# Performance work log

Hardware: AMD Instinct MI355X
Metric: run time of the kernel (lower is better)

Reference implementation:

```python
import jax, jax.numpy as jnp
import numpy as np

P = 524288          # total sampled points
N_RAYS = 4096       # rays
N_FREQ = 5
N_FREQ_VIEW = 3
ACT_SHIFT = float(np.log(1.0 / (1.0 - 0.1) - 1.0))  # alpha_init = 0.1
INTERVAL = 0.5      # stepsize * voxel_size_ratio


def sin_emb(x, n_freq):
    # x: (M,3) -> (M, 3 + 6*n_freq): [x, sin(2^i x), cos(2^i x)]
    freqs = 2.0 ** jnp.arange(n_freq, dtype=x.dtype)
    parts = [x]
    for f in freqs:
        parts.append(jnp.sin(f * x))
        parts.append(jnp.cos(f * x))
    return jnp.concatenate(parts, axis=1)


def _pipeline(sampling_coor, sampling_view, raw_density, ray_id,
              wb0, bb0, wb1, bb1, wb2, bb2,
              wa0, ba0, wa1, ba1, wa2, ba2,
              w_lat, b_lat, w_view, b_view, w_c0, b_c0, w_c1, b_c1):
    relu = jax.nn.relu
    emb = sin_emb(sampling_coor, N_FREQ)                    # (P, 33)
    view_emb = sin_emb(sampling_view, N_FREQ_VIEW)[ray_id]  # (P, 21)
    # Decoder_woslot (K == 1)
    h = relu(emb @ wb0 + bb0)
    h = relu(h @ wb1 + bb1)
    h = relu(h @ wb2 + bb2)
    h = jnp.concatenate([emb, h], axis=1)                   # skip: (P, 97)
    h = relu(h @ wa0 + ba0)
    h = relu(h @ wa1 + ba1)
    h = relu(h @ wa2 + ba2)
    latent = h @ w_lat + b_lat                              # (P, 64)
    hv = relu(jnp.concatenate([latent, view_emb], axis=1) @ w_view + b_view)
    rgb_raw = relu(hv @ w_c0 + b_c0) @ w_c1 + b_c1          # (P, 3)
    rgb = (jnp.tanh(rgb_raw) + 1.0) * 0.5
    sigma = jax.nn.softplus(raw_density[0] + ACT_SHIFT)     # (P,)
    # Raw2Alpha: alpha = 1 - exp(-sigma*interval); hence log(1-alpha) = -sigma*interval
    alpha = 1.0 - jnp.exp(-sigma * INTERVAL)
    log_t = -sigma * INTERVAL
    # Alphas2Weights: per-ray exclusive cumprod of (1-alpha); ray_id is sorted
    cl = jnp.cumsum(log_t)
    excl = cl - log_t                                        # exclusive global cumsum
    base = jax.ops.segment_max(excl, ray_id, num_segments=N_RAYS)  # value at each ray start
    T = jnp.exp(excl - base[ray_id])                         # transmittance
    weights = T * alpha                                      # (P,)
    alphainv_last = jnp.exp(jax.ops.segment_sum(log_t, ray_id, num_segments=N_RAYS))
    # composite with white background
    rgb_marched = (jax.ops.segment_sum(weights[:, None] * rgb, ray_id, num_segments=N_RAYS)
                   + alphainv_last[:, None])
    return rgb_marched                                       # (N_RAYS, 3)


def setup_inputs() -> dict:
    key = jax.random.key(0)
    ks = iter(jax.random.split(key, 40))

    def w(fi, fo):
        return jax.random.normal(next(ks), (fi, fo), jnp.float32) / np.sqrt(fi).astype(np.float32)

    inp = {
        'sampling_coor': jax.random.normal(next(ks), (P, 3), jnp.float32),
        'sampling_view': jax.random.normal(next(ks), (N_RAYS, 3), jnp.float32),
        'raw_density': jax.random.normal(next(ks), (1, P), jnp.float32),
        'ray_id': jnp.sort(jax.random.randint(next(ks), (P,), 0, N_RAYS, jnp.int32)),
        'wb0': w(33, 64), 'bb0': jnp.zeros((64,), jnp.float32),
        'wb1': w(64, 64), 'bb1': jnp.zeros((64,), jnp.float32),
        'wb2': w(64, 64), 'bb2': jnp.zeros((64,), jnp.float32),
        'wa0': w(97, 64), 'ba0': jnp.zeros((64,), jnp.float32),
        'wa1': w(64, 64), 'ba1': jnp.zeros((64,), jnp.float32),
        'wa2': w(64, 64), 'ba2': jnp.zeros((64,), jnp.float32),
        'w_lat': w(64, 64), 'b_lat': jnp.zeros((64,), jnp.float32),
        'w_view': w(85, 32), 'b_view': jnp.zeros((32,), jnp.float32),
        'w_c0': w(32, 16), 'b_c0': jnp.zeros((16,), jnp.float32),
        'w_c1': w(16, 3), 'b_c1': jnp.zeros((3,), jnp.float32),
    }
    return inp


def reference(sampling_coor, sampling_view, raw_density, ray_id,
              wb0, bb0, wb1, bb1, wb2, bb2,
              wa0, ba0, wa1, ba1, wa2, ba2,
              w_lat, b_lat, w_view, b_view, w_c0, b_c0, w_c1, b_c1):
    return _pipeline(sampling_coor, sampling_view, raw_density, ray_id,
                     wb0, bb0, wb1, bb1, wb2, bb2,
                     wa0, ba0, wa1, ba1, wa2, ba2,
                     w_lat, b_lat, w_view, b_view, w_c0, b_c0, w_c1, b_c1)
```

## Files before the change

kernel.cpp:

```cpp
#include <hip/hip_runtime.h>
#include <math.h>

#define NPTS  524288
#define NRAYS 4096
#define ACT_SHIFT_F (-2.1972245773362196f)
#define INTERVAL_F  0.5f

typedef _Float16 f16x8  __attribute__((ext_vector_type(8)));
typedef __fp16   fp16x2 __attribute__((ext_vector_type(2)));
typedef float    f32x4  __attribute__((ext_vector_type(4)));
typedef float    f32x16 __attribute__((ext_vector_type(16)));
typedef int      i32x2  __attribute__((ext_vector_type(2)));
typedef unsigned u32;
typedef unsigned u32x2  __attribute__((ext_vector_type(2)));
typedef unsigned u32x4  __attribute__((ext_vector_type(4)));

#define MFMA32(a,b,c) __builtin_amdgcn_mfma_f32_32x32x16_f16((a),(b),(c),0,0,0)

#define WB0_H    0
#define WB1_H    3328
#define WB2_H    7680
#define WA0_H    12032
#define WA1_H    19456
#define WA2_H    23808
#define WLAT_H   28160
#define WLDS_H   32512
#define WVIEW_H  32512
#define WC0_H    35584
#define WEND_H   36608
#define BTAB_H   36608
#define VTAB_H   37376
#define RAYTAB_H 168448
#define PREP_W    36608
#define PREP_BT   (PREP_W + 384)
#define PREP_IDS  (PREP_BT + NRAYS)
#define PREP_TOTAL (PREP_IDS + NPTS)

#define S2_WB0 26
#define S2_D   34
#define S2_WA0 58
#define U_WB0  0
#define U_WB1  1664
#define U_WB2  3840
#define U_WA0  6016
#define U_WA1  9728
#define U_WA2  11904
#define U_WLAT 14080
#define LDS_U32 16256

__device__ __forceinline__ u32 pk(float a, float b) {
    fp16x2 h = __builtin_amdgcn_cvt_pkrtz(a, b);
    return __builtin_bit_cast(u32, h);
}

__device__ __forceinline__ void plswap(u32 &x, u32 &y) {
    i32x2 r = __builtin_amdgcn_permlane32_swap((int)x, (int)y, false, false);
    x = (u32)r[0]; y = (u32)r[1];
}

__device__ __forceinline__ f32x16 zero16() {
    f32x16 z;
#pragma unroll
    for (int i = 0; i < 16; ++i) z[i] = 0.f;
    return z;
}

template<bool RELU>
__device__ __forceinline__ f16x8 reluq(f16x8 v) {
    if (RELU) {
        f16x8 z = {};
        return __builtin_elementwise_max(v, z);
    }
    return v;
}

template<bool RELU>
__device__ __forceinline__ void d2b(f32x16 a, f16x8 &blo, f16x8 &bhi) {
    u32 p0 = pk(a[0],a[1]),   p1 = pk(a[2],a[3]);
    u32 p2 = pk(a[4],a[5]),   p3 = pk(a[6],a[7]);
    plswap(p0, p2); plswap(p1, p3);
    u32x4 lo = {p0, p1, p2, p3};
    blo = reluq<RELU>(__builtin_bit_cast(f16x8, lo));
    u32 p4 = pk(a[8],a[9]),   p5 = pk(a[10],a[11]);
    u32 p6 = pk(a[12],a[13]), p7 = pk(a[14],a[15]);
    plswap(p4, p6); plswap(p5, p7);
    u32x4 hw = {p4, p5, p6, p7};
    bhi = reluq<RELU>(__builtin_bit_cast(f16x8, hw));
}

__device__ __forceinline__ f16x8 ldw(const u32* __restrict__ sw, int u) {
    u32x2 a = *(const u32x2*)(sw + u);
    u32x2 b = *(const u32x2*)(sw + u + 2);
    u32x4 r = {a[0], a[1], b[0], b[1]};
    return __builtin_bit_cast(f16x8, r);
}

extern "C" __global__ void __launch_bounds__(256)
prep_weights(const float* __restrict__ wb0, const float* __restrict__ bb0,
             const float* __restrict__ wb1, const float* __restrict__ bb1,
             const float* __restrict__ wb2, const float* __restrict__ bb2,
             const float* __restrict__ wa0, const float* __restrict__ ba0,
             const float* __restrict__ wa1, const float* __restrict__ ba1,
             const float* __restrict__ wa2, const float* __restrict__ ba2,
             const float* __restrict__ wlat, const float* __restrict__ blat,
             const float* __restrict__ wview, const float* __restrict__ bview,
             const float* __restrict__ wc0, const float* __restrict__ bc0,
             const float* __restrict__ view, const int* __restrict__ ray_id,
             _Float16* __restrict__ pool)
{
    const int id = blockIdx.x * 256 + threadIdx.x;
    if (id >= PREP_TOTAL) return;

    if (id < PREP_W) {
        int r = id; float v = 0.f;
        if (r < 3328) {
            int n = r / 52, k = r % 52;
            if (k < 3) v = wb0[k*64+n]; else if (k == 3) v = bb0[n];
            else if (k < 34) v = wb0[(k-1)*64+n];
        } else if (r < 7680) { r -= 3328;
            int n = r / 68, k = r % 68; if (k < 64) v = wb1[k*64+n];
        } else if (r < 12032) { r -= 7680;
            int n = r / 68, k = r % 68; if (k < 64) v = wb2[k*64+n];
        } else if (r < 19456) { r -= 12032;
            int n = r / 116, k = r % 116;
            if (k < 3) v = wa0[k*64+n]; else if (k == 3) v = ba0[n];
            else if (k < 34) v = wa0[(k-1)*64+n];
            else if (k >= 48 && k < 112) v = wa0[(k-15)*64+n];
        } else if (r < 23808) { r -= 19456;
            int n = r / 68, k = r % 68; if (k < 64) v = wa1[k*64+n];
        } else if (r < 28160) { r -= 23808;
            int n = r / 68, k = r % 68; if (k < 64) v = wa2[k*64+n];
        } else if (r < 32512) { r -= 28160;
            int n = r / 68, k = r % 68; if (k < 64) v = wlat[k*64+n];
        } else if (r < 35584) { r -= 32512;
            int n = r / 96, k = r % 96;
            if (k < 64) v = wview[k*32+n];
            else { int s = k - 64;
                   if (s < 3) v = wview[(64+s)*32+n];
                   else if (s == 3) v = bview[n];
                   else if (s < 22) v = wview[(63+s)*32+n]; }
        } else { r -= 35584;
            int n = r >> 5, k = r & 31;
            if (n < 16) v = wc0[k*16+n];
        }
        pool[id] = (_Float16)v;
        return;
    }

    if (id < PREP_BT) {
        float* bt = (float*)(pool + BTAB_H);
        const int e = id - PREP_W; float v = 0.f;
        if (e < 320) {
            int l = e >> 6, rem = e & 63;
            int mt = rem >> 5, hi2 = (rem >> 4) & 1, q = rem & 15;
            int row = (q & 3) + 8*(q >> 2) + 4*hi2 + 32*mt;
            const float* src[5] = { bb1, bb2, ba1, ba2, blat };
            v = src[l][row];
        } else if (e < 336) {
            int t = e - 320, hi2 = t >> 3, q = t & 7;
            int row = (q & 3) + 8*(q >> 2) + 4*hi2;
            v = bc0[row];
        }
        bt[e] = v;
        return;
    }

    if (id < PREP_IDS) {
        const int ray = id - PREP_BT;
        const float vx = view[3*ray+0], vy = view[3*ray+1], vz = view[3*ray+2];
        u32 w_[16];
        w_[0] = pk(vx, vy); w_[1] = pk(vz, 1.0f);
#pragma unroll
        for (int f = 0; f < 3; ++f) {
            const float fac = (float)(1 << f);
            float sx = __sinf(fac*vx), cx = __cosf(fac*vx);
            float sy = __sinf(fac*vy), cy = __cosf(fac*vy);
            float sz = __sinf(fac*vz), cz = __cosf(fac*vz);
            w_[2+3*f+0] = pk(sx,sy); w_[2+3*f+1] = pk(sz,cx); w_[2+3*f+2] = pk(cy,cz);
        }
#pragma unroll
        for (int i = 11; i < 16; ++i) w_[i] = 0u;
        u32* dst = (u32*)(pool + VTAB_H) + ray * 16;
#pragma unroll
        for (int i = 0; i < 4; ++i)
            ((u32x4*)dst)[i] = (u32x4){w_[4*i], w_[4*i+1], w_[4*i+2], w_[4*i+3]};
        return;
    }

    {
        const int p = id - PREP_IDS;
        int* tab = (int*)(pool + RAYTAB_H);
        const int cur  = ray_id[p];
        const int prev = (p == 0) ? -1 : ray_id[p-1];
        for (int r = prev + 1; r <= cur; ++r) tab[r] = p;
        if (p == NPTS - 1)
            for (int r = cur + 1; r <= NRAYS; ++r) tab[r] = NPTS;
    }
}

__device__ __forceinline__ void loadBV(f32x16 (&bv)[2], const float* __restrict__ bt,
                                       int l, int hi) {
#pragma unroll
    for (int mt = 0; mt < 2; ++mt) {
        const float* p = bt + l*64 + (mt*2 + hi)*16;
#pragma unroll
        for (int i = 0; i < 4; ++i) {
            f32x4 v = *(const f32x4*)(p + 4*i);
#pragma unroll
            for (int s = 0; s < 4; ++s) bv[mt][4*i + s] = v[s];
        }
    }
}

template<bool RELU>
__device__ __forceinline__ void denseL(const u32* __restrict__ sw, int base,
                                       const f32x16 (&bv)[2], f16x8 (&b)[4][4],
                                       int col, int hi) {
    f16x8 W[2][4];
#pragma unroll
    for (int mt = 0; mt < 2; ++mt)
#pragma unroll
        for (int kc = 0; kc < 4; ++kc)
            W[mt][kc] = ldw(sw, base + (mt*32 + col)*S2_D + kc*8 + hi*4);
#pragma unroll
    for (int t = 0; t < 4; ++t) {
        f32x16 a0 = MFMA32(W[0][0], b[t][0], bv[0]);
        f32x16 a1 = MFMA32(W[1][0], b[t][0], bv[1]);
#pragma unroll
        for (int kc = 1; kc < 4; ++kc) {
            a0 = MFMA32(W[0][kc], b[t][kc], a0);
            a1 = MFMA32(W[1][kc], b[t][kc], a1);
        }
        d2b<RELU>(a0, b[t][0], b[t][1]);
        d2b<RELU>(a1, b[t][2], b[t][3]);
    }
}

extern "C" __global__ void __launch_bounds__(512, 2)
mlp_mfma(const float* __restrict__ coor, const int* __restrict__ ray_id,
         const float* __restrict__ wc1, const float* __restrict__ bc1,
         const _Float16* __restrict__ pool, _Float16* __restrict__ rgb)
{
    __shared__ __align__(16) u32 sw[LDS_U32];
    const int tid  = threadIdx.x;
    const int lane = tid & 63;
    const int wv   = tid >> 6;
    const int col  = lane & 31;
    const int hi   = lane >> 5;
    const int wbase = blockIdx.x * 1024 + wv * 128;

    {
        const u32x4* pw = (const u32x4*)pool;
        u32x4* dw = (u32x4*)sw;
#pragma unroll
        for (int i = tid; i < LDS_U32/4; i += 512) dw[i] = pw[i];
    }

    int rid[4];
#pragma unroll
    for (int t = 0; t < 4; ++t) rid[t] = ray_id[wbase + 32*t + col];

    f16x8 E[4][3];
#pragma unroll
    for (int s = 0; s < 2; ++s) {
        const int pt = wbase + s*64 + lane;
        const float x = coor[3*pt+0], y = coor[3*pt+1], z = coor[3*pt+2];
        u32 w_[17];
        w_[0] = pk(x, y); w_[1] = pk(z, 1.0f);
#pragma unroll
        for (int f = 0; f < 5; ++f) {
            const float fac = (float)(1 << f);
            float sx = __sinf(fac*x), cx = __cosf(fac*x);
            float sy = __sinf(fac*y), cy = __cosf(fac*y);
            float sz = __sinf(fac*z), cz = __cosf(fac*z);
            w_[2+3*f+0] = pk(sx,sy); w_[2+3*f+1] = pk(sz,cx); w_[2+3*f+2] = pk(cy,cz);
        }
#pragma unroll
        for (int kc = 0; kc < 2; ++kc) {
            u32 xw[4], yw[4];
#pragma unroll
            for (int i = 0; i < 4; ++i) {
                xw[i] = w_[kc*8 + i]; yw[i] = w_[kc*8 + 4 + i];
                plswap(xw[i], yw[i]);
            }
            u32x4 lo = {xw[0], xw[1], xw[2], xw[3]};
            u32x4 hw = {yw[0], yw[1], yw[2], yw[3]};
            E[2*s  ][kc] = __builtin_bit_cast(f16x8, lo);
            E[2*s+1][kc] = __builtin_bit_cast(f16x8, hw);
        }
        u32 X = w_[16], Y = 0u;
        plswap(X, Y);
        u32x4 e2a = {X, 0u, 0u, 0u}, e2b = {Y, 0u, 0u, 0u};
        E[2*s  ][2] = __builtin_bit_cast(f16x8, e2a);
        E[2*s+1][2] = __builtin_bit_cast(f16x8, e2b);
    }
    __syncthreads();

    const float* bt = (const float*)(pool + BTAB_H);
    const f32x16 Z = zero16();

    f16x8 b[4][4];
    f32x16 bv[2];

    {
        f16x8 W[2][3];
#pragma unroll
        for (int mt = 0; mt < 2; ++mt)
#pragma unroll
            for (int kc = 0; kc < 3; ++kc)
                W[mt][kc] = ldw(sw, U_WB0 + (mt*32 + col)*S2_WB0 + kc*8 + hi*4);
#pragma unroll
        for (int t = 0; t < 4; ++t) {
            f32x16 a0 = MFMA32(W[0][0], E[t][0], Z);
            f32x16 a1 = MFMA32(W[1][0], E[t][0], Z);
            a0 = MFMA32(W[0][1], E[t][1], a0);
            a1 = MFMA32(W[1][1], E[t][1], a1);
            a0 = MFMA32(W[0][2], E[t][2], a0);
            a1 = MFMA32(W[1][2], E[t][2], a1);
            d2b<true>(a0, b[t][0], b[t][1]);
            d2b<true>(a1, b[t][2], b[t][3]);
        }
    }

    loadBV(bv, bt, 0, hi);
    denseL<true>(sw, U_WB1, bv, b, col, hi);
    loadBV(bv, bt, 1, hi);
    denseL<true>(sw, U_WB2, bv, b, col, hi);

    {
        f16x8 We[2][3], Wh[2][4];
#pragma unroll
        for (int mt = 0; mt < 2; ++mt) {
#pragma unroll
            for (int kc = 0; kc < 3; ++kc)
                We[mt][kc] = ldw(sw, U_WA0 + (mt*32 + col)*S2_WA0 + kc*8 + hi*4);
#pragma unroll
            for (int kc = 0; kc < 4; ++kc)
                Wh[mt][kc] = ldw(sw, U_WA0 + (mt*32 + col)*S2_WA0 + 24 + kc*8 + hi*4);
        }
#pragma unroll
        for (int t = 0; t < 4; ++t) {
            f32x16 a0 = MFMA32(We[0][0], E[t][0], Z);
            f32x16 a1 = MFMA32(We[1][0], E[t][0], Z);
            a0 = MFMA32(We[0][1], E[t][1], a0);
            a1 = MFMA32(We[1][1], E[t][1], a1);
            a0 = MFMA32(We[0][2], E[t][2], a0);
            a1 = MFMA32(We[1][2], E[t][2], a1);
#pragma unroll
            for (int kc = 0; kc < 4; ++kc) {
                a0 = MFMA32(Wh[0][kc], b[t][kc], a0);
                a1 = MFMA32(Wh[1][kc], b[t][kc], a1);
            }
            d2b<true>(a0, b[t][0], b[t][1]);
            d2b<true>(a1, b[t][2], b[t][3]);
        }
    }

    loadBV(bv, bt, 2, hi);
    denseL<true>(sw, U_WA1, bv, b, col, hi);
    loadBV(bv, bt, 3, hi);
    denseL<true>(sw, U_WA2, bv, b, col, hi);

    const _Float16* vtab = pool + VTAB_H;
    f16x8 VE[4][2];
#pragma unroll
    for (int t = 0; t < 4; ++t)
#pragma unroll
        for (int kc = 0; kc < 2; ++kc)
            VE[t][kc] = *(const f16x8*)(vtab + rid[t]*32 + kc*16 + hi*8);

    loadBV(bv, bt, 4, hi);
    denseL<false>(sw, U_WLAT, bv, b, col, hi);

    {
        f16x8 Wv[6];
#pragma unroll
        for (int kc = 0; kc < 6; ++kc)
            Wv[kc] = *(const f16x8*)(pool + WVIEW_H + col*96 + kc*16 + hi*8);
#pragma unroll
        for (int t = 0; t < 4; ++t) {
            f32x16 a = MFMA32(Wv[0], b[t][0], Z);
#pragma unroll
            for (int kc = 1; kc < 4; ++kc) a = MFMA32(Wv[kc], b[t][kc], a);
            a = MFMA32(Wv[4], VE[t][0], a);
            a = MFMA32(Wv[5], VE[t][1], a);
            d2b<true>(a, b[t][0], b[t][1]);
        }
    }

    {
        f16x8 Wc[2];
#pragma unroll
        for (int kc = 0; kc < 2; ++kc)
            Wc[kc] = *(const f16x8*)(pool + WC0_H + col*32 + kc*16 + hi*8);

        f32x16 C = zero16();
        {
            f32x4 c0a = *(const f32x4*)(bt + 320 + hi*8);
            f32x4 c0b = *(const f32x4*)(bt + 320 + hi*8 + 4);
#pragma unroll
            for (int s = 0; s < 4; ++s) { C[s] = c0a[s]; C[4+s] = c0b[s]; }
        }

        float wl[24];
        {
            f32x4 w0 = *(const f32x4*)(wc1 + 12*hi);
            f32x4 w1 = *(const f32x4*)(wc1 + 12*hi + 4);
            f32x4 w2 = *(const f32x4*)(wc1 + 12*hi + 8);
            f32x4 w3 = *(const f32x4*)(wc1 + 24 + 12*hi);
            f32x4 w4 = *(const f32x4*)(wc1 + 24 + 12*hi + 4);
            f32x4 w5 = *(const f32x4*)(wc1 + 24 + 12*hi + 8);
#pragma unroll
            for (int s = 0; s < 4; ++s) {
                wl[s]    = w0[s]; wl[4+s]  = w1[s]; wl[8+s]  = w2[s];
                wl[12+s] = w3[s]; wl[16+s] = w4[s]; wl[20+s] = w5[s];
            }
        }
        const float bo0 = bc1[0], bo1 = bc1[1], bo2 = bc1[2];

#pragma unroll
        for (int t = 0; t < 4; ++t) {
            f32x16 a = MFMA32(Wc[0], b[t][0], C);
            a = MFMA32(Wc[1], b[t][1], a);
            float hc[8];
#pragma unroll
            for (int i = 0; i < 8; ++i) hc[i] = fmaxf(a[i], 0.f);

            float r0 = 0.f, r1 = 0.f, r2 = 0.f;
#pragma unroll
            for (int q = 0; q < 4; ++q) {
                r0 = fmaf(hc[q], wl[3*q+0], fmaf(hc[4+q], wl[12+3*q+0], r0));
                r1 = fmaf(hc[q], wl[3*q+1], fmaf(hc[4+q], wl[12+3*q+1], r1));
                r2 = fmaf(hc[q], wl[3*q+2], fmaf(hc[4+q], wl[12+3*q+2], r2));
            }
            r0 += __shfl_xor(r0, 32);
            r1 += __shfl_xor(r1, 32);
            r2 += __shfl_xor(r2, 32);
            if (hi == 0) {
                const float K2 = 2.8853900817779268f;
                float e0 = exp2f(K2 * (r0 + bo0));
                float e1 = exp2f(K2 * (r1 + bo1));
                float e2 = exp2f(K2 * (r2 + bo2));
                float v0 = 1.f - __builtin_amdgcn_rcpf(e0 + 1.f);
                float v1 = 1.f - __builtin_amdgcn_rcpf(e1 + 1.f);
                float v2 = 1.f - __builtin_amdgcn_rcpf(e2 + 1.f);
                const int pt = wbase + 32*t + col;
                rgb[3*pt+0] = (_Float16)v0;
                rgb[3*pt+1] = (_Float16)v1;
                rgb[3*pt+2] = (_Float16)v2;
            }
        }
    }
}

extern "C" __global__ void __launch_bounds__(256)
composite(const float* __restrict__ raw_density,
          const int*   __restrict__ rtab,
          const _Float16* __restrict__ rgb,
          float*       __restrict__ out)
{
    const int lane = threadIdx.x & 63;
    const int ray  = blockIdx.x * 4 + (threadIdx.x >> 6);

    const int start = rtab[ray];
    const int end   = rtab[ray + 1];

    float carry = 0.0f, a0 = 0.0f, a1 = 0.0f, a2 = 0.0f;

    for (int base = start; base < end; base += 64) {
        const int  idx   = base + lane;
        const bool valid = idx < end;

        float lt = 0.0f, alpha = 0.0f;
        if (valid) {
            const float xx  = raw_density[idx] + ACT_SHIFT_F;
            const float sig = fmaxf(xx, 0.0f) + log1pf(expf(-fabsf(xx)));
            lt    = -sig * INTERVAL_F;
            alpha = 1.0f - expf(lt);
        }

        float incl = lt;
#pragma unroll
        for (int d = 1; d < 64; d <<= 1) {
            const float n = __shfl_up(incl, d);
            if (lane >= d) incl += n;
        }

        const float T = expf(carry + (incl - lt));
        if (valid) {
            const float w = T * alpha;
            a0 = fmaf(w, (float)rgb[3*idx+0], a0);
            a1 = fmaf(w, (float)rgb[3*idx+1], a1);
            a2 = fmaf(w, (float)rgb[3*idx+2], a2);
        }
        carry += __shfl(incl, 63);
    }

#pragma unroll
    for (int d = 32; d > 0; d >>= 1) {
        a0 += __shfl_xor(a0, d);
        a1 += __shfl_xor(a1, d);
        a2 += __shfl_xor(a2, d);
    }

    if (lane == 0) {
        const float ainv = expf(carry);
        out[3*ray+0] = a0 + ainv;
        out[3*ray+1] = a1 + ainv;
        out[3*ray+2] = a2 + ainv;
    }
}

extern "C" void kernel_launch(void* const* d_in, const int* in_sizes, int n_in,
                              void* d_out, int out_size, void* d_ws, size_t ws_size,
                              hipStream_t stream) {
    const float* coor        = (const float*)d_in[0];
    const float* view        = (const float*)d_in[1];
    const float* raw_density = (const float*)d_in[2];
    const int*   ray_id      = (const int*)  d_in[3];
    const float* wb0  = (const float*)d_in[4];  const float* bb0  = (const float*)d_in[5];
    const float* wb1  = (const float*)d_in[6];  const float* bb1  = (const float*)d_in[7];
    const float* wb2  = (const float*)d_in[8];  const float* bb2  = (const float*)d_in[9];
    const float* wa0  = (const float*)d_in[10]; const float* ba0  = (const float*)d_in[11];
    const float* wa1  = (const float*)d_in[12]; const float* ba1  = (const float*)d_in[13];
    const float* wa2  = (const float*)d_in[14]; const float* ba2  = (const float*)d_in[15];
    const float* wlat = (const float*)d_in[16]; const float* blat = (const float*)d_in[17];
    const float* wvw  = (const float*)d_in[18]; const float* bvw  = (const float*)d_in[19];
    const float* wc0  = (const float*)d_in[20]; const float* bc0  = (const float*)d_in[21];
    const float* wc1  = (const float*)d_in[22]; const float* bc1  = (const float*)d_in[23];

    _Float16* rgb  = (_Float16*)d_ws;
    _Float16* pool = (_Float16*)((char*)d_ws + (size_t)NPTS * 3 * 2);
    const int* rtab = (const int*)(pool + RAYTAB_H);

    prep_weights<<<(PREP_TOTAL + 255) / 256, 256, 0, stream>>>(
        wb0, bb0, wb1, bb1, wb2, bb2, wa0, ba0, wa1, ba1, wa2, ba2,
        wlat, blat, wvw, bvw, wc0, bc0, view, ray_id, pool);

    mlp_mfma<<<NPTS / 1024, 512, 0, stream>>>(
        coor, ray_id, wc1, bc1, pool, rgb);

    composite<<<NRAYS / 4, 256, 0, stream>>>(raw_density, rtab, rgb, (float*)d_out);
}
```

Measured before the change: 52.06 us.

## Pre-swizzle weights into per-lane MFMA fragment layout and fold biases into accumulators

```diff
diff --git a/kernel.cpp b/kernel.cpp
--- a/kernel.cpp
+++ b/kernel.cpp
@@ -12,41 +12,37 @@
 typedef float    f32x16 __attribute__((ext_vector_type(16)));
 typedef int      i32x2  __attribute__((ext_vector_type(2)));
 typedef unsigned u32;
-typedef unsigned u32x2  __attribute__((ext_vector_type(2)));
 typedef unsigned u32x4  __attribute__((ext_vector_type(4)));
 
 #define MFMA32(a,b,c) __builtin_amdgcn_mfma_f32_32x32x16_f16((a),(b),(c),0,0,0)
 
-#define WB0_H    0
-#define WB1_H    3328
-#define WB2_H    7680
-#define WA0_H    12032
-#define WA1_H    19456
-#define WA2_H    23808
-#define WLAT_H   28160
-#define WLDS_H   32512
-#define WVIEW_H  32512
-#define WC0_H    35584
-#define WEND_H   36608
-#define BTAB_H   36608
-#define VTAB_H   37376
-#define RAYTAB_H 168448
-#define PREP_W    36608
-#define PREP_BT   (PREP_W + 384)
+#define FB0_H   0
+#define FD1_H   3072
+#define FD2_H   7168
+#define FA0_H   11264
+#define FD3_H   18432
+#define FD4_H   22528
+#define FLAT_H  26624
+#define LDSW_H  30720
+#define FVIEW_H 30720
+#define FC0_H   33792
+#define BTAB_H  34816
+#define VTAB_H  35840
+#define RAYTAB_H 166912
+
+#define PREP_W    34816
+#define PREP_BT   (PREP_W + 512)
 #define PREP_IDS  (PREP_BT + NRAYS)
 #define PREP_TOTAL (PREP_IDS + NPTS)
 
-#define S2_WB0 26
-#define S2_D   34
-#define S2_WA0 58
-#define U_WB0  0
-#define U_WB1  1664
-#define U_WB2  3840
-#define U_WA0  6016
-#define U_WA1  9728
-#define U_WA2  11904
-#define U_WLAT 14080
-#define LDS_U32 16256
+#define UB0  0
+#define UD1  1536
+#define UD2  3584
+#define UA0  5632
+#define UD3  9216
+#define UD4  11264
+#define ULAT 13312
+#define LDS_U32 15360
 
 __device__ __forceinline__ u32 pk(float a, float b) {
     fp16x2 h = __builtin_amdgcn_cvt_pkrtz(a, b);
@@ -56,13 +52,6 @@
 __device__ __forceinline__ void plswap(u32 &x, u32 &y) {
     i32x2 r = __builtin_amdgcn_permlane32_swap((int)x, (int)y, false, false);
     x = (u32)r[0]; y = (u32)r[1];
-}
-
-__device__ __forceinline__ f32x16 zero16() {
-    f32x16 z;
-#pragma unroll
-    for (int i = 0; i < 16; ++i) z[i] = 0.f;
-    return z;
 }
 
 template<bool RELU>
@@ -88,11 +77,8 @@
     bhi = reluq<RELU>(__builtin_bit_cast(f16x8, hw));
 }
 
-__device__ __forceinline__ f16x8 ldw(const u32* __restrict__ sw, int u) {
-    u32x2 a = *(const u32x2*)(sw + u);
-    u32x2 b = *(const u32x2*)(sw + u + 2);
-    u32x4 r = {a[0], a[1], b[0], b[1]};
-    return __builtin_bit_cast(f16x8, r);
+__device__ __forceinline__ f16x8 ldf(const u32* __restrict__ swl, int imm) {
+    return __builtin_bit_cast(f16x8, *(const u32x4*)(swl + imm));
 }
 
 extern "C" __global__ void __launch_bounds__(256)
@@ -113,51 +99,69 @@
 
     if (id < PREP_W) {
         int r = id; float v = 0.f;
-        if (r < 3328) {
-            int n = r / 52, k = r % 52;
-            if (k < 3) v = wb0[k*64+n]; else if (k == 3) v = bb0[n];
-            else if (k < 34) v = wb0[(k-1)*64+n];
-        } else if (r < 7680) { r -= 3328;
-            int n = r / 68, k = r % 68; if (k < 64) v = wb1[k*64+n];
-        } else if (r < 12032) { r -= 7680;
-            int n = r / 68, k = r % 68; if (k < 64) v = wb2[k*64+n];
-        } else if (r < 19456) { r -= 12032;
-            int n = r / 116, k = r % 116;
-            if (k < 3) v = wa0[k*64+n]; else if (k == 3) v = ba0[n];
-            else if (k < 34) v = wa0[(k-1)*64+n];
-            else if (k >= 48 && k < 112) v = wa0[(k-15)*64+n];
-        } else if (r < 23808) { r -= 19456;
-            int n = r / 68, k = r % 68; if (k < 64) v = wa1[k*64+n];
-        } else if (r < 28160) { r -= 23808;
-            int n = r / 68, k = r % 68; if (k < 64) v = wa2[k*64+n];
-        } else if (r < 32512) { r -= 28160;
-            int n = r / 68, k = r % 68; if (k < 64) v = wlat[k*64+n];
-        } else if (r < 35584) { r -= 32512;
-            int n = r / 96, k = r % 96;
-            if (k < 64) v = wview[k*32+n];
-            else { int s = k - 64;
-                   if (s < 3) v = wview[(64+s)*32+n];
-                   else if (s == 3) v = bview[n];
-                   else if (s < 22) v = wview[(63+s)*32+n]; }
-        } else { r -= 35584;
-            int n = r >> 5, k = r & 31;
-            if (n < 16) v = wc0[k*16+n];
-        }
-        pool[id] = (_Float16)v;
+        if (r < 33792) {
+            const float* W; int base, MT;
+            if      (r < 3072)  { W = wb0;  base = 0;     MT = 2; }
+            else if (r < 7168)  { W = wb1;  base = 3072;  MT = 2; }
+            else if (r < 11264) { W = wb2;  base = 7168;  MT = 2; }
+            else if (r < 18432) { W = wa0;  base = 11264; MT = 2; }
+            else if (r < 22528) { W = wa1;  base = 18432; MT = 2; }
+            else if (r < 26624) { W = wa2;  base = 22528; MT = 2; }
+            else if (r < 30720) { W = wlat; base = 26624; MT = 2; }
+            else                { W = wview;base = 30720; MT = 1; }
+            const int e    = r - base;
+            const int j    = e & 7;
+            const int lane = (e >> 3) & 63;
+            const int col  = lane & 31, hi = lane >> 5;
+            int kc, mt;
+            if (MT == 2) { kc = e >> 10; mt = (e >> 9) & 1; }
+            else         { kc = e >> 9;  mt = 0; }
+            const int of = mt * 32 + col;
+            const int k  = kc * 16 + hi * 8 + j;
+            if (W == wb0) {
+                if (k < 3) v = wb0[k*64+of];
+                else if (k >= 4 && k < 34) v = wb0[(k-1)*64+of];
+            } else if (W == wa0) {
+                if (k < 3) v = wa0[k*64+of];
+                else if (k >= 4 && k < 34) v = wa0[(k-1)*64+of];
+                else if (k >= 48 && k < 112) v = wa0[(k-15)*64+of];
+            } else if (W == wview) {
+                if (k < 64) v = wview[k*32+of];
+                else { int s = k - 64;
+                       if (s < 3) v = wview[(64+s)*32+of];
+                       else if (s >= 4 && s < 22) v = wview[(63+s)*32+of]; }
+            } else {
+                if (k < 64) v = W[k*64+of];
+            }
+            pool[id] = (_Float16)v;
+        } else {
+            const int e = r - 33792;
+            const int j = e & 7;
+            const int lane = (e >> 3) & 63;
+            const int col = lane & 31, hi = lane >> 5;
+            const int kc = e >> 9;
+            const int k = kc * 16 + hi * 8 + j;
+            float v2 = (col < 16 && k < 32) ? wc0[k*16+col] : 0.f;
+            pool[id] = (_Float16)v2;
+        }
         return;
     }
 
     if (id < PREP_BT) {
         float* bt = (float*)(pool + BTAB_H);
         const int e = id - PREP_W; float v = 0.f;
-        if (e < 320) {
+        if (e < 448) {
             int l = e >> 6, rem = e & 63;
             int mt = rem >> 5, hi2 = (rem >> 4) & 1, q = rem & 15;
             int row = (q & 3) + 8*(q >> 2) + 4*hi2 + 32*mt;
-            const float* src[5] = { bb1, bb2, ba1, ba2, blat };
+            const float* src[7] = { bb0, bb1, bb2, ba0, ba1, ba2, blat };
             v = src[l][row];
-        } else if (e < 336) {
-            int t = e - 320, hi2 = t >> 3, q = t & 7;
+        } else if (e < 480) {
+            int t = e - 448, hi2 = t >> 4, q = t & 15;
+            int row = (q & 3) + 8*(q >> 2) + 4*hi2;
+            v = bview[row];
+        } else if (e < 496) {
+            int t = e - 480, hi2 = t >> 3, q = t & 7;
             int row = (q & 3) + 8*(q >> 2) + 4*hi2;
             v = bc0[row];
         }
@@ -169,7 +173,7 @@
         const int ray = id - PREP_BT;
         const float vx = view[3*ray+0], vy = view[3*ray+1], vz = view[3*ray+2];
         u32 w_[16];
-        w_[0] = pk(vx, vy); w_[1] = pk(vz, 1.0f);
+        w_[0] = pk(vx, vy); w_[1] = pk(vz, 0.f);
 #pragma unroll
         for (int f = 0; f < 3; ++f) {
             const float fac = (float)(1 << f);
@@ -213,15 +217,14 @@
 }
 
 template<bool RELU>
-__device__ __forceinline__ void denseL(const u32* __restrict__ sw, int base,
-                                       const f32x16 (&bv)[2], f16x8 (&b)[4][4],
-                                       int col, int hi) {
+__device__ __forceinline__ void denseL(const u32* __restrict__ swl, int base,
+                                       const f32x16 (&bv)[2], f16x8 (&b)[4][4]) {
     f16x8 W[2][4];
 #pragma unroll
     for (int mt = 0; mt < 2; ++mt)
 #pragma unroll
         for (int kc = 0; kc < 4; ++kc)
-            W[mt][kc] = ldw(sw, base + (mt*32 + col)*S2_D + kc*8 + hi*4);
+            W[mt][kc] = ldf(swl, base + (kc*2 + mt)*256);
 #pragma unroll
     for (int t = 0; t < 4; ++t) {
         f32x16 a0 = MFMA32(W[0][0], b[t][0], bv[0]);
@@ -266,7 +269,7 @@
         const int pt = wbase + s*64 + lane;
         const float x = coor[3*pt+0], y = coor[3*pt+1], z = coor[3*pt+2];
         u32 w_[17];
-        w_[0] = pk(x, y); w_[1] = pk(z, 1.0f);
+        w_[0] = pk(x, y); w_[1] = pk(z, 0.f);
 #pragma unroll
         for (int f = 0; f < 5; ++f) {
             const float fac = (float)(1 << f);
@@ -296,8 +299,8 @@
     }
     __syncthreads();
 
+    const u32* swl = sw + lane * 4;
     const float* bt = (const float*)(pool + BTAB_H);
-    const f32x16 Z = zero16();
 
     f16x8 b[4][4];
     f32x16 bv[2];
@@ -308,11 +311,12 @@
         for (int mt = 0; mt < 2; ++mt)
 #pragma unroll
             for (int kc = 0; kc < 3; ++kc)
-                W[mt][kc] = ldw(sw, U_WB0 + (mt*32 + col)*S2_WB0 + kc*8 + hi*4);
+                W[mt][kc] = ldf(swl, UB0 + (kc*2 + mt)*256);
+        loadBV(bv, bt, 0, hi);
 #pragma unroll
         for (int t = 0; t < 4; ++t) {
-            f32x16 a0 = MFMA32(W[0][0], E[t][0], Z);
-            f32x16 a1 = MFMA32(W[1][0], E[t][0], Z);
+            f32x16 a0 = MFMA32(W[0][0], E[t][0], bv[0]);
+            f32x16 a1 = MFMA32(W[1][0], E[t][0], bv[1]);
             a0 = MFMA32(W[0][1], E[t][1], a0);
             a1 = MFMA32(W[1][1], E[t][1], a1);
             a0 = MFMA32(W[0][2], E[t][2], a0);
@@ -322,10 +326,10 @@
         }
     }
 
-    loadBV(bv, bt, 0, hi);
-    denseL<true>(sw, U_WB1, bv, b, col, hi);
     loadBV(bv, bt, 1, hi);
-    denseL<true>(sw, U_WB2, bv, b, col, hi);
+    denseL<true>(swl, UD1, bv, b);
+    loadBV(bv, bt, 2, hi);
+    denseL<true>(swl, UD2, bv, b);
 
     {
         f16x8 We[2][3], Wh[2][4];
@@ -333,15 +337,16 @@
         for (int mt = 0; mt < 2; ++mt) {
 #pragma unroll
             for (int kc = 0; kc < 3; ++kc)
-                We[mt][kc] = ldw(sw, U_WA0 + (mt*32 + col)*S2_WA0 + kc*8 + hi*4);
+                We[mt][kc] = ldf(swl, UA0 + (kc*2 + mt)*256);
 #pragma unroll
             for (int kc = 0; kc < 4; ++kc)
-                Wh[mt][kc] = ldw(sw, U_WA0 + (mt*32 + col)*S2_WA0 + 24 + kc*8 + hi*4);
-        }
+                Wh[mt][kc] = ldf(swl, UA0 + ((kc+3)*2 + mt)*256);
+        }
+        loadBV(bv, bt, 3, hi);
 #pragma unroll
         for (int t = 0; t < 4; ++t) {
-            f32x16 a0 = MFMA32(We[0][0], E[t][0], Z);
-            f32x16 a1 = MFMA32(We[1][0], E[t][0], Z);
+            f32x16 a0 = MFMA32(We[0][0], E[t][0], bv[0]);
+            f32x16 a1 = MFMA32(We[1][0], E[t][0], bv[1]);
             a0 = MFMA32(We[0][1], E[t][1], a0);
             a1 = MFMA32(We[1][1], E[t][1], a1);
             a0 = MFMA32(We[0][2], E[t][2], a0);
@@ -356,10 +361,10 @@
         }
     }
 
-    loadBV(bv, bt, 2, hi);
-    denseL<true>(sw, U_WA1, bv, b, col, hi);
-    loadBV(bv, bt, 3, hi);
-    denseL<true>(sw, U_WA2, bv, b, col, hi);
+    loadBV(bv, bt, 4, hi);
+    denseL<true>(swl, UD3, bv, b);
+    loadBV(bv, bt, 5, hi);
+    denseL<true>(swl, UD4, bv, b);
 
     const _Float16* vtab = pool + VTAB_H;
     f16x8 VE[4][2];
@@ -369,17 +374,27 @@
         for (int kc = 0; kc < 2; ++kc)
             VE[t][kc] = *(const f16x8*)(vtab + rid[t]*32 + kc*16 + hi*8);
 
-    loadBV(bv, bt, 4, hi);
-    denseL<false>(sw, U_WLAT, bv, b, col, hi);
+    loadBV(bv, bt, 6, hi);
+    denseL<false>(swl, ULAT, bv, b);
 
     {
         f16x8 Wv[6];
 #pragma unroll
         for (int kc = 0; kc < 6; ++kc)
-            Wv[kc] = *(const f16x8*)(pool + WVIEW_H + col*96 + kc*16 + hi*8);
+            Wv[kc] = *(const f16x8*)(pool + FVIEW_H + (kc*64 + lane)*8);
+        f32x16 bvv;
+        {
+            const float* p = bt + 448 + hi*16;
+#pragma unroll
+            for (int i = 0; i < 4; ++i) {
+                f32x4 v = *(const f32x4*)(p + 4*i);
+#pragma unroll
+                for (int s = 0; s < 4; ++s) bvv[4*i + s] = v[s];
+            }
+        }
 #pragma unroll
         for (int t = 0; t < 4; ++t) {
-            f32x16 a = MFMA32(Wv[0], b[t][0], Z);
+            f32x16 a = MFMA32(Wv[0], b[t][0], bvv);
 #pragma unroll
             for (int kc = 1; kc < 4; ++kc) a = MFMA32(Wv[kc], b[t][kc], a);
             a = MFMA32(Wv[4], VE[t][0], a);
@@ -392,14 +407,16 @@
         f16x8 Wc[2];
 #pragma unroll
         for (int kc = 0; kc < 2; ++kc)
-            Wc[kc] = *(const f16x8*)(pool + WC0_H + col*32 + kc*16 + hi*8);
-
-        f32x16 C = zero16();
+            Wc[kc] = *(const f16x8*)(pool + FC0_H + (kc*64 + lane)*8);
+
+        f32x16 C;
         {
-            f32x4 c0a = *(const f32x4*)(bt + 320 + hi*8);
-            f32x4 c0b = *(const f32x4*)(bt + 320 + hi*8 + 4);
-#pragma unroll
-            for (int s = 0; s < 4; ++s) { C[s] = c0a[s]; C[4+s] = c0b[s]; }
+            f32x4 c0a = *(const f32x4*)(bt + 480 + hi*8);
+            f32x4 c0b = *(const f32x4*)(bt + 480 + hi*8 + 4);
+#pragma unroll
+            for (int s = 0; s < 4; ++s) {
+                C[s] = c0a[s]; C[4+s] = c0b[s]; C[8+s] = 0.f; C[12+s] = 0.f;
+            }
         }
 
         float wl[24];
```

Measured after the change: 52.01 us. No clear change (-0.1%).
